# Kernel optimization log

Measured on AMD Instinct MI355X. Metric: run time of the kernel, lower is better.

## Reference

```python
import jax, jax.numpy as jnp
import numpy as np

N = 8192
NEG = -1e9  # masked-logit fill (finite to stay fp16/bf16-safe)


def _gat_layer(x, W, a_src, a_dst, adj, apply_elu):
    # x: [N, Fin], W: [Fin, Fout]
    h = x @ W                                   # [N, Fout]
    f_src = h @ a_src                           # [N] attention contribution of source i
    f_dst = h @ a_dst                           # [N] attention contribution of target j
    e = jax.nn.leaky_relu(f_src[:, None] + f_dst[None, :], negative_slope=0.2)  # [N, N]
    e = jnp.where(adj > 0, e, NEG)
    attn = jax.nn.softmax(e, axis=1)            # masked neighbor softmax per node
    out = attn @ h                              # [N, Fout]
    return jax.nn.elu(out) if apply_elu else out


def setup_inputs() -> dict:
    key = jax.random.key(0)
    ks = jax.random.split(key, 8)
    x = jax.random.normal(ks[0], (N, 512), dtype=jnp.float32)
    E_rand = 262144
    ei = jax.random.randint(ks[1], (2, E_rand), 0, N, dtype=jnp.int64)
    loops = jnp.broadcast_to(jnp.arange(N, dtype=jnp.int64), (2, N))
    edge_index = jnp.concatenate([ei, loops], axis=1)  # self-loops avoid empty softmax rows
    W1 = jax.random.normal(ks[2], (512, 256), dtype=jnp.float32) * (1.0 / np.sqrt(512))
    a1_src = jax.random.normal(ks[3], (256,), dtype=jnp.float32) * 0.1
    a1_dst = jax.random.normal(ks[4], (256,), dtype=jnp.float32) * 0.1
    W2 = jax.random.normal(ks[5], (256, 16), dtype=jnp.float32) * (1.0 / np.sqrt(256))
    a2_src = jax.random.normal(ks[6], (16,), dtype=jnp.float32) * 0.1
    a2_dst = jax.random.normal(ks[7], (16,), dtype=jnp.float32) * 0.1
    return {"x": x, "edge_index": edge_index, "W1": W1, "a1_src": a1_src,
            "a1_dst": a1_dst, "W2": W2, "a2_src": a2_src, "a2_dst": a2_dst}


def reference(x, edge_index, W1, a1_src, a1_dst, W2, a2_src, a2_dst):
    # dense adjacency scatter, exactly as the torch module does
    adj = jnp.zeros((N, N), dtype=x.dtype).at[edge_index[0], edge_index[1]].set(1.0)
    # inference: dropout disabled
    h = _gat_layer(x, W1, a1_src, a1_dst, adj, apply_elu=True)
    logits = _gat_layer(h, W2, a2_src, a2_dst, adj, apply_elu=False)
    return jax.nn.log_softmax(logits, axis=1)
```

## Files before the change

kernel.cpp:

```cpp
#include <hip/hip_runtime.h>
#include <hip/hip_bf16.h>


#define NN 8192
#define MAXD 128

typedef __bf16 bf16x8 __attribute__((ext_vector_type(8)));
typedef float f32x4 __attribute__((ext_vector_type(4)));
typedef unsigned short u16x8 __attribute__((ext_vector_type(8)));

__device__ __forceinline__ unsigned short f2bf(float f) {
  unsigned u = __float_as_uint(f);
  unsigned r = (u + 0x7fffu + ((u >> 16) & 1u)) >> 16;
  return (unsigned short)r;
}
__device__ __forceinline__ float bf2f(unsigned short u) {
  return __uint_as_float(((unsigned)u) << 16);
}
__device__ __forceinline__ float lrelu02(float e) { return e > 0.f ? e : 0.2f * e; }

__global__ __launch_bounds__(256) void prep_kernel(uint4* __restrict__ bitmap,
                                                   const float* __restrict__ W1,
                                                   unsigned short* __restrict__ W1t,
                                                   const float* __restrict__ W2,
                                                   unsigned short* __restrict__ W2t) {
  const int bid = blockIdx.x, tid = threadIdx.x;
  if (bid < 2048) {
    bitmap[bid * 256 + tid] = uint4{0u, 0u, 0u, 0u};
  } else if (bid < 2560) {
    const int gid = (bid - 2048) * 256 + tid;
    const int n = gid >> 9, k = gid & 511;
    W1t[gid] = f2bf(W1[(size_t)k * 256 + n]);
  } else {
    for (int i = tid; i < 16 * 256; i += 256) {
      const int n = i >> 8, k = i & 255;
      W2t[i] = f2bf(W2[(size_t)k * 16 + n]);
    }
  }
}

__global__ __launch_bounds__(256) void gemm1_mfma_kernel(
    const float* __restrict__ X, const unsigned short* __restrict__ W1t,
    unsigned short* __restrict__ h1b) {
  constexpr int K = 512;
  __shared__ __align__(16) unsigned short lds[(128 * 64) + (64 * 64)];
  const int t = threadIdx.x;
  const int w = t >> 6, l = t & 63;
  const int bm = blockIdx.x * 128, bn = blockIdx.y * 64;
  const int r8 = t >> 3, c8 = t & 7;

  f32x4 acc[2][4];
  const f32x4 fz = {0.f, 0.f, 0.f, 0.f};
#pragma unroll
  for (int i = 0; i < 2; ++i)
#pragma unroll
    for (int j = 0; j < 4; ++j) acc[i][j] = fz;

  for (int k0 = 0; k0 < K; k0 += 64) {
    float4 xa[4][2];
#pragma unroll
    for (int p = 0; p < 4; ++p) {
      const float* s = X + (size_t)(bm + r8 + p * 32) * K + k0 + c8 * 8;
      xa[p][0] = *(const float4*)s;
      xa[p][1] = *(const float4*)(s + 4);
    }
    uint4 wb[2];
#pragma unroll
    for (int p = 0; p < 2; ++p)
      wb[p] = *(const uint4*)(W1t + (size_t)(bn + r8 + p * 32) * K + k0 + c8 * 8);
    __syncthreads();
#pragma unroll
    for (int p = 0; p < 4; ++p) {
      const int row = r8 + p * 32;
      const int u = ((row >> 4) << 7) + ((c8 >> 2) << 6) + ((c8 & 3) << 4) + (row & 15);
      u16x8 v;
      v[0] = f2bf(xa[p][0].x); v[1] = f2bf(xa[p][0].y);
      v[2] = f2bf(xa[p][0].z); v[3] = f2bf(xa[p][0].w);
      v[4] = f2bf(xa[p][1].x); v[5] = f2bf(xa[p][1].y);
      v[6] = f2bf(xa[p][1].z); v[7] = f2bf(xa[p][1].w);
      *(u16x8*)(lds + u * 8) = v;
    }
#pragma unroll
    for (int p = 0; p < 2; ++p) {
      const int col = r8 + p * 32;
      const int u = 1024 + ((col >> 4) << 7) + ((c8 >> 2) << 6) + ((c8 & 3) << 4) + (col & 15);
      *(uint4*)(lds + u * 8) = wb[p];
    }
    __syncthreads();
#pragma unroll
    for (int ks = 0; ks < 2; ++ks) {
      const bf16x8 a0 = *(const bf16x8*)(lds + ((w * 2 + 0) * 128 + ks * 64 + l) * 8);
      const bf16x8 a1 = *(const bf16x8*)(lds + ((w * 2 + 1) * 128 + ks * 64 + l) * 8);
      const bf16x8 b0 = *(const bf16x8*)(lds + (1024 + 0 * 128 + ks * 64 + l) * 8);
      const bf16x8 b1 = *(const bf16x8*)(lds + (1024 + 1 * 128 + ks * 64 + l) * 8);
      const bf16x8 b2 = *(const bf16x8*)(lds + (1024 + 2 * 128 + ks * 64 + l) * 8);
      const bf16x8 b3 = *(const bf16x8*)(lds + (1024 + 3 * 128 + ks * 64 + l) * 8);
      acc[0][0] = __builtin_amdgcn_mfma_f32_16x16x32_bf16(a0, b0, acc[0][0], 0, 0, 0);
      acc[0][1] = __builtin_amdgcn_mfma_f32_16x16x32_bf16(a0, b1, acc[0][1], 0, 0, 0);
      acc[0][2] = __builtin_amdgcn_mfma_f32_16x16x32_bf16(a0, b2, acc[0][2], 0, 0, 0);
      acc[0][3] = __builtin_amdgcn_mfma_f32_16x16x32_bf16(a0, b3, acc[0][3], 0, 0, 0);
      acc[1][0] = __builtin_amdgcn_mfma_f32_16x16x32_bf16(a1, b0, acc[1][0], 0, 0, 0);
      acc[1][1] = __builtin_amdgcn_mfma_f32_16x16x32_bf16(a1, b1, acc[1][1], 0, 0, 0);
      acc[1][2] = __builtin_amdgcn_mfma_f32_16x16x32_bf16(a1, b2, acc[1][2], 0, 0, 0);
      acc[1][3] = __builtin_amdgcn_mfma_f32_16x16x32_bf16(a1, b3, acc[1][3], 0, 0, 0);
    }
  }
#pragma unroll
  for (int i = 0; i < 2; ++i)
#pragma unroll
    for (int j = 0; j < 4; ++j)
#pragma unroll
      for (int q = 0; q < 4; ++q) {
        const int row = bm + w * 32 + i * 16 + (l >> 4) * 4 + q;
        const int col = bn + j * 16 + (l & 15);
        h1b[(size_t)row * 256 + col] = f2bf(acc[i][j][q]);
      }
}

__global__ __launch_bounds__(256) void f1_kernel(const unsigned short* __restrict__ h1b,
                                                 const float* __restrict__ a_src,
                                                 const float* __restrict__ a_dst,
                                                 float* __restrict__ fs,
                                                 float* __restrict__ fd) {
  const int lane = threadIdx.x & 63;
  const int row = blockIdx.x * 4 + (threadIdx.x >> 6);
  const ushort4 hv = *(const ushort4*)(h1b + (size_t)row * 256 + lane * 4);
  const float h0 = bf2f(hv.x), h1 = bf2f(hv.y), h2 = bf2f(hv.z), h3 = bf2f(hv.w);
  const float4 as = *(const float4*)(a_src + lane * 4);
  const float4 ad = *(const float4*)(a_dst + lane * 4);
  float ss = h0 * as.x + h1 * as.y + h2 * as.z + h3 * as.w;
  float dd = h0 * ad.x + h1 * ad.y + h2 * ad.z + h3 * ad.w;
#pragma unroll
  for (int off = 32; off; off >>= 1) {
    ss += __shfl_xor(ss, off);
    dd += __shfl_xor(dd, off);
  }
  if (lane == 0) {
    fs[row] = ss;
    fd[row] = dd;
  }
}

__global__ void scatter_kernel(const int* __restrict__ ei, int E,
                               unsigned* __restrict__ bitmap) {
  const int t = blockIdx.x * 256 + threadIdx.x;
  if (t >= E) return;
  const int s = ei[t];
  const int d = ei[E + t];
  atomicOr(bitmap + (size_t)s * 256 + (d >> 5), 1u << (d & 31));
}

__global__ __launch_bounds__(256) void build_csr_kernel(unsigned* __restrict__ bitmap,
                                                        int* __restrict__ deg) {
  const int lane = threadIdx.x & 63;
  const int row = blockIdx.x * 4 + (threadIdx.x >> 6);
  unsigned* brow = bitmap + (size_t)row * 256;
  const uint4 wv = *(const uint4*)(brow + lane * 4);
  const int cnt = __popc(wv.x) + __popc(wv.y) + __popc(wv.z) + __popc(wv.w);
  int inc = cnt;
#pragma unroll
  for (int d = 1; d < 64; d <<= 1) {
    const int t = __shfl_up(inc, d);
    if (lane >= d) inc += t;
  }
  int off = inc - cnt;
  const int total = __shfl(inc, 63);
  unsigned short* nb = (unsigned short*)brow;
  const unsigned words[4] = {wv.x, wv.y, wv.z, wv.w};
  const int base_j = lane * 128;
#pragma unroll
  for (int q = 0; q < 4; ++q) {
    unsigned word = words[q];
    while (word) {
      const int b = __ffs(word) - 1;
      word &= word - 1;
      nb[off++] = (unsigned short)(base_j + q * 32 + b);
    }
  }
  if (lane == 0) deg[row] = total;
}

__global__ __launch_bounds__(256) void attn1_kernel(const unsigned* __restrict__ bitmap,
                                                    const int* __restrict__ degarr,
                                                    const unsigned short* __restrict__ h1b,
                                                    const float* __restrict__ fs,
                                                    const float* __restrict__ fd,
                                                    unsigned short* __restrict__ out1b) {
  __shared__ float wsh[4][MAXD];
  __shared__ int jsh[4][MAXD];
  const int lane = threadIdx.x & 63;
  const int wv = threadIdx.x >> 6;
  const int row = blockIdx.x * 4 + wv;
  const unsigned short* nb = (const unsigned short*)(bitmap + (size_t)row * 256);
  const int deg = degarr[row];
  const float fsr = fs[row];
  const int j0 = (lane < deg) ? (int)nb[lane] : 0;
  const int j1 = (lane + 64 < deg) ? (int)nb[lane + 64] : 0;
  const float e0 = (lane < deg) ? lrelu02(fsr + fd[j0]) : -1e30f;
  const float e1 = (lane + 64 < deg) ? lrelu02(fsr + fd[j1]) : -1e30f;
  float m = fmaxf(e0, e1);
#pragma unroll
  for (int off = 32; off; off >>= 1) m = fmaxf(m, __shfl_xor(m, off));
  const float w0 = (lane < deg) ? expf(e0 - m) : 0.f;
  const float w1 = (lane + 64 < deg) ? expf(e1 - m) : 0.f;
  float s = w0 + w1;
#pragma unroll
  for (int off = 32; off; off >>= 1) s += __shfl_xor(s, off);
  wsh[wv][lane] = w0;
  jsh[wv][lane] = j0;
  wsh[wv][lane + 64] = w1;
  jsh[wv][lane + 64] = j1;
  float4 acc = {0.f, 0.f, 0.f, 0.f};
  int t = 0;
  for (; t + 4 <= deg; t += 4) {
    const float W0 = wsh[wv][t], W1 = wsh[wv][t + 1], W2 = wsh[wv][t + 2], W3 = wsh[wv][t + 3];
    const int J0 = jsh[wv][t], J1 = jsh[wv][t + 1], J2 = jsh[wv][t + 2], J3 = jsh[wv][t + 3];
    const ushort4 v0 = *(const ushort4*)(h1b + (size_t)J0 * 256 + lane * 4);
    const ushort4 v1 = *(const ushort4*)(h1b + (size_t)J1 * 256 + lane * 4);
    const ushort4 v2 = *(const ushort4*)(h1b + (size_t)J2 * 256 + lane * 4);
    const ushort4 v3 = *(const ushort4*)(h1b + (size_t)J3 * 256 + lane * 4);
    acc.x = fmaf(W0, bf2f(v0.x), fmaf(W1, bf2f(v1.x), fmaf(W2, bf2f(v2.x), fmaf(W3, bf2f(v3.x), acc.x))));
    acc.y = fmaf(W0, bf2f(v0.y), fmaf(W1, bf2f(v1.y), fmaf(W2, bf2f(v2.y), fmaf(W3, bf2f(v3.y), acc.y))));
    acc.z = fmaf(W0, bf2f(v0.z), fmaf(W1, bf2f(v1.z), fmaf(W2, bf2f(v2.z), fmaf(W3, bf2f(v3.z), acc.z))));
    acc.w = fmaf(W0, bf2f(v0.w), fmaf(W1, bf2f(v1.w), fmaf(W2, bf2f(v2.w), fmaf(W3, bf2f(v3.w), acc.w))));
  }
  for (; t < deg; ++t) {
    const float W0 = wsh[wv][t];
    const int J0 = jsh[wv][t];
    const ushort4 v0 = *(const ushort4*)(h1b + (size_t)J0 * 256 + lane * 4);
    acc.x = fmaf(W0, bf2f(v0.x), acc.x);
    acc.y = fmaf(W0, bf2f(v0.y), acc.y);
    acc.z = fmaf(W0, bf2f(v0.z), acc.z);
    acc.w = fmaf(W0, bf2f(v0.w), acc.w);
  }
  const float inv = 1.f / s;
  float4 v = {acc.x * inv, acc.y * inv, acc.z * inv, acc.w * inv};
  v.x = v.x > 0.f ? v.x : expf(v.x) - 1.f;
  v.y = v.y > 0.f ? v.y : expf(v.y) - 1.f;
  v.z = v.z > 0.f ? v.z : expf(v.z) - 1.f;
  v.w = v.w > 0.f ? v.w : expf(v.w) - 1.f;
  ushort4 o;
  o.x = f2bf(v.x); o.y = f2bf(v.y); o.z = f2bf(v.z); o.w = f2bf(v.w);
  *(ushort4*)(out1b + (size_t)row * 256 + lane * 4) = o;
}

__global__ __launch_bounds__(256) void gemm2f2_kernel(
    const unsigned short* __restrict__ out1b, const unsigned short* __restrict__ W2t,
    const float* __restrict__ a2s, const float* __restrict__ a2d,
    float* __restrict__ h2, float* __restrict__ fs, float* __restrict__ fd) {
  const int l = threadIdx.x & 63, w = threadIdx.x >> 6;
  const int row0 = blockIdx.x * 64 + w * 16;
  const int lr = l & 15, lg = l >> 4;
  f32x4 acc = {0.f, 0.f, 0.f, 0.f};
#pragma unroll
  for (int k0 = 0; k0 < 256; k0 += 32) {
    const bf16x8 a = *(const bf16x8*)(out1b + (size_t)(row0 + lr) * 256 + k0 + lg * 8);
    const bf16x8 b = *(const bf16x8*)(W2t + (size_t)lr * 256 + k0 + lg * 8);
    acc = __builtin_amdgcn_mfma_f32_16x16x32_bf16(a, b, acc, 0, 0, 0);
  }
  const float as = a2s[lr], ad = a2d[lr];
#pragma unroll
  for (int q = 0; q < 4; ++q) {
    const int row = row0 + lg * 4 + q;
    const float v = acc[q];
    h2[(size_t)row * 16 + lr] = v;
    float ss = v * as, dd = v * ad;
#pragma unroll
    for (int off = 8; off; off >>= 1) {
      ss += __shfl_xor(ss, off, 16);
      dd += __shfl_xor(dd, off, 16);
    }
    if (lr == 0) {
      fs[row] = ss;
      fd[row] = dd;
    }
  }
}

__global__ __launch_bounds__(256) void attn2_kernel(const unsigned* __restrict__ bitmap,
                                                    const int* __restrict__ degarr,
                                                    const float* __restrict__ h2,
                                                    const float* __restrict__ fs,
                                                    const float* __restrict__ fd,
                                                    float* __restrict__ out) {
  __shared__ float wsh[4][MAXD];
  __shared__ int jsh[4][MAXD];
  const int lane = threadIdx.x & 63;
  const int wv = threadIdx.x >> 6;
  const int row = blockIdx.x * 4 + wv;
  const unsigned short* nb = (const unsigned short*)(bitmap + (size_t)row * 256);
  const int deg = degarr[row];
  const float fsr = fs[row];
  const int j0 = (lane < deg) ? (int)nb[lane] : 0;
  const int j1 = (lane + 64 < deg) ? (int)nb[lane + 64] : 0;
  const float e0 = (lane < deg) ? lrelu02(fsr + fd[j0]) : -1e30f;
  const float e1 = (lane + 64 < deg) ? lrelu02(fsr + fd[j1]) : -1e30f;
  float m = fmaxf(e0, e1);
#pragma unroll
  for (int off = 32; off; off >>= 1) m = fmaxf(m, __shfl_xor(m, off));
  const float w0 = (lane < deg) ? expf(e0 - m) : 0.f;
  const float w1 = (lane + 64 < deg) ? expf(e1 - m) : 0.f;
  float s = w0 + w1;
#pragma unroll
  for (int off = 32; off; off >>= 1) s += __shfl_xor(s, off);
  wsh[wv][lane] = w0;
  jsh[wv][lane] = j0;
  wsh[wv][lane + 64] = w1;
  jsh[wv][lane + 64] = j1;
  const int c = lane & 15, g = lane >> 4;
  float acc = 0.f;
  int t = g;
  for (; t + 4 < deg; t += 8) {
    const float W0 = wsh[wv][t], W1 = wsh[wv][t + 4];
    const float v0 = h2[(size_t)jsh[wv][t] * 16 + c];
    const float v1 = h2[(size_t)jsh[wv][t + 4] * 16 + c];
    acc = fmaf(W0, v0, fmaf(W1, v1, acc));
  }
  if (t < deg) acc = fmaf(wsh[wv][t], h2[(size_t)jsh[wv][t] * 16 + c], acc);
  acc += __shfl_xor(acc, 16);
  acc += __shfl_xor(acc, 32);
  const float v = acc / s;
  float mx = v;
#pragma unroll
  for (int off = 8; off; off >>= 1) mx = fmaxf(mx, __shfl_xor(mx, off, 16));
  float se = expf(v - mx);
#pragma unroll
  for (int off = 8; off; off >>= 1) se += __shfl_xor(se, off, 16);
  if (lane < 16) out[(size_t)row * 16 + lane] = v - mx - logf(se);
}

extern "C" void kernel_launch(void* const* d_in, const int* in_sizes, int n_in,
                              void* d_out, int out_size, void* d_ws, size_t ws_size,
                              hipStream_t stream) {
  const float* x = (const float*)d_in[0];
  const int* ei = (const int*)d_in[1];
  const float* W1 = (const float*)d_in[2];
  const float* a1s = (const float*)d_in[3];
  const float* a1d = (const float*)d_in[4];
  const float* W2 = (const float*)d_in[5];
  const float* a2s = (const float*)d_in[6];
  const float* a2d = (const float*)d_in[7];
  float* out = (float*)d_out;
  const int E = in_sizes[1] / 2;

  char* ws = (char*)d_ws;
  unsigned short* h1b = (unsigned short*)ws;
  unsigned short* out1b = (unsigned short*)(ws + (4u << 20));
  unsigned* bitmap = (unsigned*)(ws + (16u << 20));
  float* f1s = (float*)(ws + (24u << 20));
  float* f1d = f1s + NN;
  float* h2 = f1d + NN;
  float* f2s = h2 + (size_t)NN * 16;
  float* f2d = f2s + NN;
  int* deg = (int*)(f2d + NN);
  unsigned short* w1t = (unsigned short*)(deg + NN);
  unsigned short* w2t = w1t + (size_t)256 * 512;

  prep_kernel<<<2561, 256, 0, stream>>>((uint4*)bitmap, W1, w1t, W2, w2t);
  scatter_kernel<<<(E + 255) / 256, 256, 0, stream>>>(ei, E, bitmap);
  build_csr_kernel<<<NN / 4, 256, 0, stream>>>(bitmap, deg);
  gemm1_mfma_kernel<<<dim3(NN / 128, 256 / 64), 256, 0, stream>>>(x, w1t, h1b);
  f1_kernel<<<NN / 4, 256, 0, stream>>>(h1b, a1s, a1d, f1s, f1d);
  attn1_kernel<<<NN / 4, 256, 0, stream>>>(bitmap, deg, h1b, f1s, f1d, out1b);
  gemm2f2_kernel<<<NN / 64, 256, 0, stream>>>(out1b, w2t, a2s, a2d, h2, f2s, f2d);
  attn2_kernel<<<NN / 4, 256, 0, stream>>>(bitmap, deg, h2, f2s, f2d, out);
}
```

Measured before the change: 78.54 us.

## Fuse f1 projection into GEMM1 epilogue and widen attention gather loads

```diff
diff --git a/kernel.cpp b/kernel.cpp
--- a/kernel.cpp
+++ b/kernel.cpp
@@ -23,7 +23,8 @@
                                                    const float* __restrict__ W1,
                                                    unsigned short* __restrict__ W1t,
                                                    const float* __restrict__ W2,
-                                                   unsigned short* __restrict__ W2t) {
+                                                   unsigned short* __restrict__ W2t,
+                                                   float4* __restrict__ f1sd) {
   const int bid = blockIdx.x, tid = threadIdx.x;
   if (bid < 2048) {
     bitmap[bid * 256 + tid] = uint4{0u, 0u, 0u, 0u};
@@ -31,17 +32,20 @@
     const int gid = (bid - 2048) * 256 + tid;
     const int n = gid >> 9, k = gid & 511;
     W1t[gid] = f2bf(W1[(size_t)k * 256 + n]);
-  } else {
+  } else if (bid == 2560) {
     for (int i = tid; i < 16 * 256; i += 256) {
       const int n = i >> 8, k = i & 255;
       W2t[i] = f2bf(W2[(size_t)k * 16 + n]);
     }
+  } else {
+    for (int i = tid; i < 4096; i += 256) f1sd[i] = float4{0.f, 0.f, 0.f, 0.f};
   }
 }
 
 __global__ __launch_bounds__(256) void gemm1_mfma_kernel(
     const float* __restrict__ X, const unsigned short* __restrict__ W1t,
-    unsigned short* __restrict__ h1b) {
+    unsigned short* __restrict__ h1b, const float* __restrict__ A1S,
+    const float* __restrict__ A1D, float* __restrict__ f1s, float* __restrict__ f1d) {
   constexpr int K = 512;
   __shared__ __align__(16) unsigned short lds[(128 * 64) + (64 * 64)];
   const int t = threadIdx.x;
@@ -115,30 +119,34 @@
         const int col = bn + j * 16 + (l & 15);
         h1b[(size_t)row * 256 + col] = f2bf(acc[i][j][q]);
       }
-}
-
-__global__ __launch_bounds__(256) void f1_kernel(const unsigned short* __restrict__ h1b,
-                                                 const float* __restrict__ a_src,
-                                                 const float* __restrict__ a_dst,
-                                                 float* __restrict__ fs,
-                                                 float* __restrict__ fd) {
-  const int lane = threadIdx.x & 63;
-  const int row = blockIdx.x * 4 + (threadIdx.x >> 6);
-  const ushort4 hv = *(const ushort4*)(h1b + (size_t)row * 256 + lane * 4);
-  const float h0 = bf2f(hv.x), h1 = bf2f(hv.y), h2 = bf2f(hv.z), h3 = bf2f(hv.w);
-  const float4 as = *(const float4*)(a_src + lane * 4);
-  const float4 ad = *(const float4*)(a_dst + lane * 4);
-  float ss = h0 * as.x + h1 * as.y + h2 * as.z + h3 * as.w;
-  float dd = h0 * ad.x + h1 * ad.y + h2 * ad.z + h3 * ad.w;
-#pragma unroll
-  for (int off = 32; off; off >>= 1) {
-    ss += __shfl_xor(ss, off);
-    dd += __shfl_xor(dd, off);
-  }
-  if (lane == 0) {
-    fs[row] = ss;
-    fd[row] = dd;
-  }
+  const int lc = l & 15;
+  float a1sv[4], a1dv[4];
+#pragma unroll
+  for (int j = 0; j < 4; ++j) {
+    a1sv[j] = A1S[bn + j * 16 + lc];
+    a1dv[j] = A1D[bn + j * 16 + lc];
+  }
+#pragma unroll
+  for (int i = 0; i < 2; ++i)
+#pragma unroll
+    for (int q = 0; q < 4; ++q) {
+      float ps = 0.f, pd = 0.f;
+#pragma unroll
+      for (int j = 0; j < 4; ++j) {
+        ps = fmaf(acc[i][j][q], a1sv[j], ps);
+        pd = fmaf(acc[i][j][q], a1dv[j], pd);
+      }
+#pragma unroll
+      for (int off = 8; off; off >>= 1) {
+        ps += __shfl_xor(ps, off, 16);
+        pd += __shfl_xor(pd, off, 16);
+      }
+      if (lc == 0) {
+        const int row = bm + w * 32 + i * 16 + (l >> 4) * 4 + q;
+        atomicAdd(f1s + row, ps);
+        atomicAdd(f1d + row, pd);
+      }
+    }
 }
 
 __global__ void scatter_kernel(const int* __restrict__ ei, int E,
@@ -210,38 +218,42 @@
   jsh[wv][lane] = j0;
   wsh[wv][lane + 64] = w1;
   jsh[wv][lane + 64] = j1;
-  float4 acc = {0.f, 0.f, 0.f, 0.f};
+  const int half = lane >> 5, lh = lane & 31;
+  float acc[8] = {0.f, 0.f, 0.f, 0.f, 0.f, 0.f, 0.f, 0.f};
   int t = 0;
-  for (; t + 4 <= deg; t += 4) {
-    const float W0 = wsh[wv][t], W1 = wsh[wv][t + 1], W2 = wsh[wv][t + 2], W3 = wsh[wv][t + 3];
-    const int J0 = jsh[wv][t], J1 = jsh[wv][t + 1], J2 = jsh[wv][t + 2], J3 = jsh[wv][t + 3];
-    const ushort4 v0 = *(const ushort4*)(h1b + (size_t)J0 * 256 + lane * 4);
-    const ushort4 v1 = *(const ushort4*)(h1b + (size_t)J1 * 256 + lane * 4);
-    const ushort4 v2 = *(const ushort4*)(h1b + (size_t)J2 * 256 + lane * 4);
-    const ushort4 v3 = *(const ushort4*)(h1b + (size_t)J3 * 256 + lane * 4);
-    acc.x = fmaf(W0, bf2f(v0.x), fmaf(W1, bf2f(v1.x), fmaf(W2, bf2f(v2.x), fmaf(W3, bf2f(v3.x), acc.x))));
-    acc.y = fmaf(W0, bf2f(v0.y), fmaf(W1, bf2f(v1.y), fmaf(W2, bf2f(v2.y), fmaf(W3, bf2f(v3.y), acc.y))));
-    acc.z = fmaf(W0, bf2f(v0.z), fmaf(W1, bf2f(v1.z), fmaf(W2, bf2f(v2.z), fmaf(W3, bf2f(v3.z), acc.z))));
-    acc.w = fmaf(W0, bf2f(v0.w), fmaf(W1, bf2f(v1.w), fmaf(W2, bf2f(v2.w), fmaf(W3, bf2f(v3.w), acc.w))));
-  }
-  for (; t < deg; ++t) {
-    const float W0 = wsh[wv][t];
-    const int J0 = jsh[wv][t];
-    const ushort4 v0 = *(const ushort4*)(h1b + (size_t)J0 * 256 + lane * 4);
-    acc.x = fmaf(W0, bf2f(v0.x), acc.x);
-    acc.y = fmaf(W0, bf2f(v0.y), acc.y);
-    acc.z = fmaf(W0, bf2f(v0.z), acc.z);
-    acc.w = fmaf(W0, bf2f(v0.w), acc.w);
-  }
+  for (; t + 8 <= deg; t += 8) {
+    const int ja = jsh[wv][t + half], jb = jsh[wv][t + 2 + half];
+    const int jc = jsh[wv][t + 4 + half], jd = jsh[wv][t + 6 + half];
+    const float Wa = wsh[wv][t + half], Wb = wsh[wv][t + 2 + half];
+    const float Wc = wsh[wv][t + 4 + half], Wd = wsh[wv][t + 6 + half];
+    const u16x8 va = *(const u16x8*)(h1b + (size_t)ja * 256 + lh * 8);
+    const u16x8 vb = *(const u16x8*)(h1b + (size_t)jb * 256 + lh * 8);
+    const u16x8 vc = *(const u16x8*)(h1b + (size_t)jc * 256 + lh * 8);
+    const u16x8 vd = *(const u16x8*)(h1b + (size_t)jd * 256 + lh * 8);
+#pragma unroll
+    for (int e = 0; e < 8; ++e)
+      acc[e] = fmaf(Wa, bf2f(va[e]),
+               fmaf(Wb, bf2f(vb[e]), fmaf(Wc, bf2f(vc[e]), fmaf(Wd, bf2f(vd[e]), acc[e]))));
+  }
+  for (; t < deg; t += 2) {
+    const int idx = t + half;
+    const int jt = (idx < deg) ? jsh[wv][idx] : 0;
+    const float Wt = (idx < deg) ? wsh[wv][idx] : 0.f;
+    const u16x8 v = *(const u16x8*)(h1b + (size_t)jt * 256 + lh * 8);
+#pragma unroll
+    for (int e = 0; e < 8; ++e) acc[e] = fmaf(Wt, bf2f(v[e]), acc[e]);
+  }
+#pragma unroll
+  for (int e = 0; e < 8; ++e) acc[e] += __shfl_xor(acc[e], 32);
   const float inv = 1.f / s;
-  float4 v = {acc.x * inv, acc.y * inv, acc.z * inv, acc.w * inv};
-  v.x = v.x > 0.f ? v.x : expf(v.x) - 1.f;
-  v.y = v.y > 0.f ? v.y : expf(v.y) - 1.f;
-  v.z = v.z > 0.f ? v.z : expf(v.z) - 1.f;
-  v.w = v.w > 0.f ? v.w : expf(v.w) - 1.f;
-  ushort4 o;
-  o.x = f2bf(v.x); o.y = f2bf(v.y); o.z = f2bf(v.z); o.w = f2bf(v.w);
-  *(ushort4*)(out1b + (size_t)row * 256 + lane * 4) = o;
+  u16x8 o;
+#pragma unroll
+  for (int e = 0; e < 8; ++e) {
+    float v = acc[e] * inv;
+    v = v > 0.f ? v : expf(v) - 1.f;
+    o[e] = f2bf(v);
+  }
+  if (lane < 32) *(u16x8*)(out1b + (size_t)row * 256 + lh * 8) = o;
 }
 
 __global__ __launch_bounds__(256) void gemm2f2_kernel(
@@ -310,13 +322,16 @@
   const int c = lane & 15, g = lane >> 4;
   float acc = 0.f;
   int t = g;
-  for (; t + 4 < deg; t += 8) {
+  for (; t + 12 < deg; t += 16) {
     const float W0 = wsh[wv][t], W1 = wsh[wv][t + 4];
+    const float W2 = wsh[wv][t + 8], W3 = wsh[wv][t + 12];
     const float v0 = h2[(size_t)jsh[wv][t] * 16 + c];
     const float v1 = h2[(size_t)jsh[wv][t + 4] * 16 + c];
-    acc = fmaf(W0, v0, fmaf(W1, v1, acc));
-  }
-  if (t < deg) acc = fmaf(wsh[wv][t], h2[(size_t)jsh[wv][t] * 16 + c], acc);
+    const float v2 = h2[(size_t)jsh[wv][t + 8] * 16 + c];
+    const float v3 = h2[(size_t)jsh[wv][t + 12] * 16 + c];
+    acc = fmaf(W0, v0, fmaf(W1, v1, fmaf(W2, v2, fmaf(W3, v3, acc))));
+  }
+  for (; t < deg; t += 4) acc = fmaf(wsh[wv][t], h2[(size_t)jsh[wv][t] * 16 + c], acc);
   acc += __shfl_xor(acc, 16);
   acc += __shfl_xor(acc, 32);
   const float v = acc / s;
@@ -356,11 +371,11 @@
   unsigned short* w1t = (unsigned short*)(deg + NN);
   unsigned short* w2t = w1t + (size_t)256 * 512;
 
-  prep_kernel<<<2561, 256, 0, stream>>>((uint4*)bitmap, W1, w1t, W2, w2t);
+  prep_kernel<<<2562, 256, 0, stream>>>((uint4*)bitmap, W1, w1t, W2, w2t, (float4*)f1s);
   scatter_kernel<<<(E + 255) / 256, 256, 0, stream>>>(ei, E, bitmap);
   build_csr_kernel<<<NN / 4, 256, 0, stream>>>(bitmap, deg);
-  gemm1_mfma_kernel<<<dim3(NN / 128, 256 / 64), 256, 0, stream>>>(x, w1t, h1b);
-  f1_kernel<<<NN / 4, 256, 0, stream>>>(h1b, a1s, a1d, f1s, f1d);
+  gemm1_mfma_kernel<<<dim3(NN / 128, 256 / 64), 256, 0, stream>>>(x, w1t, h1b, a1s, a1d,
+                                                                  f1s, f1d);
   attn1_kernel<<<NN / 4, 256, 0, stream>>>(bitmap, deg, h1b, f1s, f1d, out1b);
   gemm2f2_kernel<<<NN / 64, 256, 0, stream>>>(out1b, w2t, a2s, a2d, h2, f2s, f2d);
   attn2_kernel<<<NN / 4, 256, 0, stream>>>(bitmap, deg, h2, f2s, f2d, out);
```

After: 74.96 us. 1.05x faster.
